# Kernel tuning notes

Measured on AMD Instinct MI355X. Metric: run time of the kernel, lower is better.

The kernel has to match this reference:

```python
import jax, jax.numpy as jnp
import numpy as np

N_RES = 500000


def _rot(vals):
    # stack 9 scalars-per-element into (..., 3, 3) row-major rotation matrices
    return jnp.stack(vals, axis=-1).reshape(*vals[0].shape, 3, 3)


def _dihedral(p0, p1, p2, p3):
    b0 = -(p1 - p0)
    b1 = p2 - p1
    b2 = p3 - p2
    b0xb1 = jnp.cross(b0, b1)
    b1xb2 = jnp.cross(b2, b1)
    y = jnp.sum(jnp.cross(b0xb1, b1xb2) * b1, axis=-1) / jnp.linalg.norm(b1, axis=-1)
    x = jnp.sum(b0xb1 * b1xb2, axis=-1)
    return jnp.nan_to_num(jnp.arctan2(y, x))


def _bb_dihedrals(N, CA, C):
    phi_ = _dihedral(C[:-1], N[1:], CA[1:], C[1:])
    psi_ = _dihedral(N[:-1], CA[:-1], C[:-1], N[1:])
    omg_ = _dihedral(CA[:-1], C[:-1], N[1:], CA[1:])
    pad = jnp.zeros_like(phi_[:1])
    omega = jnp.concatenate([omg_, pad])
    phi = jnp.concatenate([pad, phi_])
    psi = jnp.concatenate([psi_, pad])
    return jnp.stack([omega, phi, psi], axis=-1)  # (n, 3)


def _frames_from_reference(n_xyz, ca_xyz, c_xyz, eps=1e-20):
    # OpenFold Rigid.make_transform_from_reference
    n = n_xyz - ca_xyz
    c = c_xyz - ca_xyz
    cx, cy, cz = c[..., 0], c[..., 1], c[..., 2]
    z = jnp.zeros_like(cx)
    o = jnp.ones_like(cx)
    nrm = jnp.sqrt(eps + cx**2 + cy**2)
    s1, c1 = -cy / nrm, cx / nrm
    R1 = _rot([c1, -s1, z, s1, c1, z, z, z, o])
    nrm2 = jnp.sqrt(eps + cx**2 + cy**2 + cz**2)
    s2, c2 = cz / nrm2, jnp.sqrt(cx**2 + cy**2) / nrm2
    R2 = _rot([c2, z, s2, z, o, z, -s2, z, c2])
    Rc = R2 @ R1
    n2 = jnp.einsum('...ij,...j->...i', Rc, n)
    ny, nz_ = n2[..., 1], n2[..., 2]
    nrm3 = jnp.sqrt(eps + ny**2 + nz_**2)
    sn, cn = -nz_ / nrm3, ny / nrm3
    Rn = _rot([o, z, z, z, cn, -sn, z, sn, cn])
    rots = jnp.swapaxes(Rn @ Rc, -1, -2)
    return rots, ca_xyz  # (n,3,3), (n,3)


def _compose(ra, ta, rb, tb):
    # rigid composition: (ra,ta) o (rb,tb)
    return ra @ rb, jnp.einsum('...ij,...j->...i', ra, tb) + ta


def _forward(aa, bb_coords, sc_torsions, default_frames, group_idx, atom_mask, lit_positions):
    n_xyz, ca_xyz, c_xyz = bb_coords[:, 0], bb_coords[:, 1], bb_coords[:, 2]
    bb_r, bb_t = _frames_from_reference(n_xyz, ca_xyz, c_xyz)

    angles = jnp.concatenate([_bb_dihedrals(n_xyz, ca_xyz, c_xyz), sc_torsions], axis=-1)  # (n,7)
    alpha = jnp.stack([jnp.sin(angles), jnp.cos(angles)], axis=-1)  # (n,7,2) [sin, cos]
    bb_pad = jnp.concatenate([
        jnp.zeros((alpha.shape[0], 1, 1), alpha.dtype),
        jnp.ones((alpha.shape[0], 1, 1), alpha.dtype)], axis=-1)
    alpha = jnp.concatenate([bb_pad, alpha], axis=-2)  # (n,8,2)

    # torsion_angles_to_frames
    d4 = default_frames[aa]            # (n,8,4,4)
    dr, dt = d4[..., :3, :3], d4[..., :3, 3]
    s, cA = alpha[..., 0], alpha[..., 1]
    z = jnp.zeros_like(s)
    o = jnp.ones_like(s)
    Ra = _rot([o, z, z, z, cA, -s, z, s, cA])  # (n,8,3,3) x-axis rotation
    fr = dr @ Ra
    ft = dt
    # chain chi2->chi1, chi3->chi2, chi4->chi3
    r2, t2 = _compose(fr[:, 4], ft[:, 4], fr[:, 5], ft[:, 5])
    r3, t3 = _compose(r2, t2, fr[:, 6], ft[:, 6])
    r4, t4 = _compose(r3, t3, fr[:, 7], ft[:, 7])
    all_r = jnp.concatenate([fr[:, :5], r2[:, None], r3[:, None], r4[:, None]], axis=1)
    all_t = jnp.concatenate([ft[:, :5], t2[:, None], t3[:, None], t4[:, None]], axis=1)
    gr, gt = _compose(bb_r[:, None], bb_t[:, None], all_r, all_t)  # (n,8,3,3), (n,8,3)

    # frames_and_literature_positions_to_atom14_pos (one-hot sum == gather)
    n = aa.shape[0]
    g = group_idx[aa]                   # (n,14)
    ridx = jnp.arange(n)[:, None]
    ar = gr[ridx, g]                    # (n,14,3,3)
    at = gt[ridx, g]                    # (n,14,3)
    lit = lit_positions[aa]             # (n,14,3)
    pred = jnp.einsum('naij,naj->nai', ar, lit) + at
    pred = pred * atom_mask[aa][..., None]

    # use_native_bb_coords=True: keep input backbone atoms
    return jnp.concatenate([bb_coords, pred[:, 4:]], axis=1)  # (n,14,3)


def setup_inputs() -> dict:
    key = jax.random.key(0)
    ks = jax.random.split(key, 7)
    n = N_RES
    aa = jax.random.randint(ks[0], (n,), 0, 21, dtype=jnp.int32)
    bb_coords = jax.random.normal(ks[1], (n, 4, 3), jnp.float32) * 3.0
    sc_torsions = jax.random.uniform(ks[2], (n, 4), jnp.float32, -np.pi, np.pi)
    default_frames = jax.random.normal(ks[3], (21, 8, 4, 4), jnp.float32)
    group_idx = jax.random.randint(ks[4], (21, 14), 0, 8, dtype=jnp.int32)
    atom_mask = (jax.random.uniform(ks[5], (21, 14)) > 0.2).astype(jnp.float32)
    lit_positions = jax.random.normal(ks[6], (21, 14, 3), jnp.float32)
    return {"aa": aa, "bb_coords": bb_coords, "sc_torsions": sc_torsions,
            "default_frames": default_frames, "group_idx": group_idx,
            "atom_mask": atom_mask, "lit_positions": lit_positions}


def reference(aa, bb_coords, sc_torsions, default_frames, group_idx, atom_mask, lit_positions):
    return _forward(aa, bb_coords, sc_torsions, default_frames, group_idx, atom_mask, lit_positions)
```

## Files before the change

kernel.cpp:

```cpp
#include <hip/hip_runtime.h>
#include <hip/hip_fp16.h>


struct F3 { float x, y, z; };

__device__ __forceinline__ F3 f3sub(F3 a, F3 b) { return {a.x-b.x, a.y-b.y, a.z-b.z}; }
__device__ __forceinline__ F3 f3cross(F3 a, F3 b) {
    return {a.y*b.z - a.z*b.y, a.z*b.x - a.x*b.z, a.x*b.y - a.y*b.x};
}
__device__ __forceinline__ float f3dot(F3 a, F3 b) { return a.x*b.x + a.y*b.y + a.z*b.z; }

__device__ __forceinline__ void dihedral_from(F3 A, F3 B, F3 mid,
                                              float& s, float& c) {
    float x = f3dot(A, B);
    F3 w = f3cross(A, B);
    float y = f3dot(w, mid) * rsqrtf(fmaxf(f3dot(mid, mid), 1e-30f));
    float r2 = x * x + y * y;
    float rinv = rsqrtf(r2);
    bool ok = r2 > 1e-24f;
    s = ok ? y * rinv : 0.0f;
    c = ok ? x * rinv : 1.0f;
}

struct Xf12 { float m[9]; float t[3]; };
__device__ __forceinline__ Xf12 mk_fr(float4 r0, float4 r1, float4 r2,
                                      float sA, float cA) {
    Xf12 o;
    o.m[0] = r0.x; o.m[1] = fmaf(cA, r0.y, sA * r0.z); o.m[2] = fmaf(cA, r0.z, -sA * r0.y);
    o.m[3] = r1.x; o.m[4] = fmaf(cA, r1.y, sA * r1.z); o.m[5] = fmaf(cA, r1.z, -sA * r1.y);
    o.m[6] = r2.x; o.m[7] = fmaf(cA, r2.y, sA * r2.z); o.m[8] = fmaf(cA, r2.z, -sA * r2.y);
    o.t[0] = r0.w; o.t[1] = r1.w; o.t[2] = r2.w;
    return o;
}

__device__ __forceinline__ void cond_apply(const Xf12& F, bool cond,
                                           float& qx, float& qy, float& qz) {
    float tx = fmaf(F.m[0], qx, fmaf(F.m[1], qy, fmaf(F.m[2], qz, F.t[0])));
    float ty = fmaf(F.m[3], qx, fmaf(F.m[4], qy, fmaf(F.m[5], qz, F.t[1])));
    float tz = fmaf(F.m[6], qx, fmaf(F.m[7], qy, fmaf(F.m[8], qz, F.t[2])));
    qx = cond ? tx : qx; qy = cond ? ty : qy; qz = cond ? tz : qz;
}

__device__ __forceinline__ float2 h2f(float packed) {
    __half2 h = *reinterpret_cast<__half2*>(&packed);
    return __half22float2(h);
}

#define OT_STRIDE 34
#define AUV_AA    62

__global__ __launch_bounds__(256)
__attribute__((amdgpu_waves_per_eu(2, 4)))
void idealizer_kernel(
    const int*   __restrict__ aa,
    const float* __restrict__ bb,
    const float* __restrict__ tor,
    const float* __restrict__ dframes,
    const int*   __restrict__ gidx,
    const float* __restrict__ amask,
    const float* __restrict__ lit,
    float*       __restrict__ out,
    int n)
{
    __shared__ __align__(16) float s_ot[256 * OT_STRIDE];
    __shared__ __align__(16) float s_auv[21 * AUV_AA];
    __shared__ unsigned s_gpk[21];
    __shared__ unsigned s_mbit[21];

    const int tid = threadIdx.x;

    if (tid < 210) {
        int aai = (tid * 6554) >> 16;
        int a   = tid - aai * 10;
        int g   = gidx[aai * 14 + 4 + a];
        const float4* dr4 = (const float4*)dframes + (aai * 8 + g) * 4;
        float4 d0 = dr4[0], d1 = dr4[1], d2 = dr4[2];
        const float* lp = lit + aai * 42 + 12 + a * 3;
        float lx = lp[0], ly = lp[1], lz = lp[2];
        float* w = &s_auv[aai * AUV_AA + a * 6];
        w[0] = fmaf(d0.x, lx, d0.w);
        w[1] = fmaf(d1.x, lx, d1.w);
        w[2] = fmaf(d2.x, lx, d2.w);
        float U0 = fmaf(d0.y, ly, d0.z * lz), V0 = fmaf(d0.z, ly, -d0.y * lz);
        float U1 = fmaf(d1.y, ly, d1.z * lz), V1 = fmaf(d1.z, ly, -d1.y * lz);
        float U2 = fmaf(d2.y, ly, d2.z * lz), V2 = fmaf(d2.z, ly, -d2.y * lz);
        ((__half2*)w)[3] = __floats2half2_rn(U0, U1);
        ((__half2*)w)[4] = __floats2half2_rn(U2, V0);
        ((__half2*)w)[5] = __floats2half2_rn(V1, V2);
    }
    if (tid < 21) {
        unsigned gp = 0, mb = 0;
        #pragma unroll
        for (int a = 0; a < 10; a++) {
            gp |= ((unsigned)gidx[tid * 14 + 4 + a]) << (3 * a);
            mb |= (amask[tid * 14 + 4 + a] != 0.0f ? 1u : 0u) << a;
        }
        s_gpk[tid] = gp;
        s_mbit[tid] = mb;
    }
    __syncthreads();

    const int i0 = blockIdx.x * 256;
    const int i  = i0 + tid;
    if (i < n) {
        const int aai = aa[i];
        const float4* bb4 = (const float4*)bb;
        float4 q0 = bb4[i * 3 + 0];
        float4 q1 = bb4[i * 3 + 1];
        float Cz  = bb[i * 12 + 8];
        const int im = (i > 0)     ? i - 1 : 0;
        const int ip = (i < n - 1) ? i + 1 : 0;
        float4 t1 = bb4[im * 3 + 1];
        float  t2 = bb[im * 12 + 8];
        float4 r0 = bb4[ip * 3 + 0];
        float2 r1 = ((const float2*)bb)[ip * 6 + 2];
        float4 tv = ((const float4*)tor)[i];
        const float4* dfp = (const float4*)dframes + (aai * 32 + 16);
        float4 e40 = dfp[0], e41 = dfp[1],  e42 = dfp[2];
        float4 e50 = dfp[4], e51 = dfp[5],  e52 = dfp[6];
        float4 e60 = dfp[8], e61 = dfp[9],  e62 = dfp[10];

        const unsigned gpk  = s_gpk[aai];
        const unsigned mbit = s_mbit[aai];

        F3 Np  = {q0.x, q0.y, q0.z};
        F3 CAp = {q0.w, q1.x, q1.y};
        F3 Cp  = {q1.z, q1.w, Cz};
        F3 Cm  = {t1.z, t1.w, t2};
        F3 Nn  = {r0.x, r0.y, r0.z};
        F3 CAn = {r0.w, r1.x, r1.y};

        F3 u1 = f3sub(Np, Cm);
        F3 u2 = f3sub(CAp, Np);
        F3 u3 = f3sub(Cp, CAp);
        F3 u4 = f3sub(Nn, Cp);
        F3 u5 = f3sub(CAn, Nn);
        F3 c12 = f3cross(u1, u2), c23 = f3cross(u2, u3);
        F3 c34 = f3cross(u3, u4), c45 = f3cross(u4, u5);
        float s_ph, c_ph, s_ps, c_ps, s_om, c_om;
        dihedral_from(c12, c23, u2, s_ph, c_ph);
        dihedral_from(c23, c34, u3, s_ps, c_ps);
        dihedral_from(c34, c45, u4, s_om, c_om);
        if (i == 0)     { s_ph = 0.0f; c_ph = 1.0f; }
        if (i == n - 1) { s_ps = 0.0f; c_ps = 1.0f; s_om = 0.0f; c_om = 1.0f; }

        const float eps = 1e-20f;
        F3 nv = f3sub(Np, CAp);
        F3 cv = f3sub(Cp, CAp);
        float cx = cv.x, cy = cv.y, cz2 = cv.z;
        float d2xy  = cx * cx + cy * cy;
        float inrm  = rsqrtf(eps + d2xy);
        float s1 = -cy * inrm, c1 = cx * inrm;
        float inrm2 = rsqrtf(eps + d2xy + cz2 * cz2);
        float s2v = cz2 * inrm2, c2v = sqrtf(d2xy) * inrm2;
        float Rc00 = c2v * c1,  Rc01 = -c2v * s1, Rc02 = s2v;
        float Rc10 = s1,        Rc11 = c1,        Rc12 = 0.0f;
        float Rc20 = -s2v * c1, Rc21 = s2v * s1,  Rc22 = c2v;
        float n2y = Rc10 * nv.x + Rc11 * nv.y + Rc12 * nv.z;
        float n2z = Rc20 * nv.x + Rc21 * nv.y + Rc22 * nv.z;
        float inrm3 = rsqrtf(eps + n2y * n2y + n2z * n2z);
        float sn = -n2z * inrm3, cn = n2y * inrm3;
        float M10 = cn * Rc10 - sn * Rc20, M11 = cn * Rc11 - sn * Rc21, M12 = cn * Rc12 - sn * Rc22;
        float M20 = sn * Rc10 + cn * Rc20, M21 = sn * Rc11 + cn * Rc21;
        float M22 = sn * Rc12 + cn * Rc22;
        float B00 = Rc00, B01 = M10, B02 = M20;
        float B10 = Rc01, B11 = M11, B12 = M21;
        float B20 = Rc02, B21 = M12, B22 = M22;

        float sang[8], cang[8];
        sang[0] = 0.0f; cang[0] = 1.0f;
        sang[1] = s_om; cang[1] = c_om;
        sang[2] = s_ph; cang[2] = c_ph;
        sang[3] = s_ps; cang[3] = c_ps;
        __sincosf(tv.x, &sang[4], &cang[4]);
        __sincosf(tv.y, &sang[5], &cang[5]);
        __sincosf(tv.z, &sang[6], &cang[6]);
        __sincosf(tv.w, &sang[7], &cang[7]);

        float* row = &s_ot[tid * OT_STRIDE];
        float2* scw = (float2*)(row + 18);
        #pragma unroll
        for (int g8 = 0; g8 < 8; g8++)
            scw[g8] = make_float2(sang[g8], cang[g8]);

        const Xf12 F4 = mk_fr(e40, e41, e42, sang[4], cang[4]);
        const Xf12 F5 = mk_fr(e50, e51, e52, sang[5], cang[5]);
        const Xf12 F6 = mk_fr(e60, e61, e62, sang[6], cang[6]);

        float v[30];
        const float* auv = &s_auv[aai * AUV_AA];
        #pragma unroll
        for (int a = 0; a < 10; a++) {
            int g = (gpk >> (3 * a)) & 7;
            float2 sc = *(const float2*)(row + 18 + 2 * g);
            const float* ap = auv + a * 6;
            float2 w0 = *(const float2*)ap;
            float2 w1 = *(const float2*)(ap + 2);
            float2 w2 = *(const float2*)(ap + 4);
            float2 u01  = h2f(w1.y);
            float2 u2v0 = h2f(w2.x);
            float2 v12  = h2f(w2.y);
            float qx = fmaf(sc.y, u01.x,  fmaf(sc.x, u2v0.y, w0.x));
            float qy = fmaf(sc.y, u01.y,  fmaf(sc.x, v12.x,  w0.y));
            float qz = fmaf(sc.y, u2v0.x, fmaf(sc.x, v12.y,  w1.x));
            cond_apply(F6, g >= 7, qx, qy, qz);
            cond_apply(F5, g >= 6, qx, qy, qz);
            cond_apply(F4, g >= 5, qx, qy, qz);
            float mk = ((mbit >> a) & 1u) ? 1.0f : 0.0f;
            v[3*a]   = mk * fmaf(B00, qx, fmaf(B01, qy, fmaf(B02, qz, CAp.x)));
            v[3*a+1] = mk * fmaf(B10, qx, fmaf(B11, qy, fmaf(B12, qz, CAp.y)));
            v[3*a+2] = mk * fmaf(B20, qx, fmaf(B21, qy, fmaf(B22, qz, CAp.z)));
        }

        float2* so2 = (float2*)row;
        #pragma unroll
        for (int k = 0; k < 15; k++)
            so2[k] = make_float2(v[2*k], v[2*k+1]);
    }

    __syncthreads();

    int m = n - i0; if (m > 256) m = 256;
    float2* gout = (float2*)(out + (size_t)i0 * 42);
    const float2* bbt = (const float2*)(bb + (size_t)i0 * 12);
    if (m == 256) {
        int r = (tid * 24967) >> 19;
        int j = tid - r * 21;
        #pragma unroll
        for (int k = 0; k < 21; k++) {
            int off = tid + (k << 8);
            int bi = (j < 6) ? (r * 6 + j) : 0;
            float2 gval = bbt[bi];
            int tj = (j < 6) ? 0 : (j - 6);
            const float* tp = &s_ot[r * OT_STRIDE + 2 * tj];
            float2 lval = make_float2(tp[0], tp[1]);
            gout[off] = (j < 6) ? gval : lval;
            r += 12; j += 4;
            if (j >= 21) { j -= 21; r += 1; }
        }
    } else {
        const int cnt2 = m * 21;
        int r = tid / 21;
        int j = tid - r * 21;
        for (int off = tid; off < cnt2; off += 256) {
            int bi = (j < 6) ? (r * 6 + j) : 0;
            float2 gval = bbt[bi];
            int tj = (j < 6) ? 0 : (j - 6);
            const float* tp = &s_ot[r * OT_STRIDE + 2 * tj];
            float2 lval = make_float2(tp[0], tp[1]);
            gout[off] = (j < 6) ? gval : lval;
            r += 12; j += 4;
            if (j >= 21) { j -= 21; r += 1; }
        }
    }
}

extern "C" void kernel_launch(void* const* d_in, const int* in_sizes, int n_in,
                              void* d_out, int out_size, void* d_ws, size_t ws_size,
                              hipStream_t stream) {
    const int*   aa  = (const int*)d_in[0];
    const float* bb  = (const float*)d_in[1];
    const float* tor = (const float*)d_in[2];
    const float* df  = (const float*)d_in[3];
    const int*   gi  = (const int*)d_in[4];
    const float* am  = (const float*)d_in[5];
    const float* lp  = (const float*)d_in[6];
    float* outp = (float*)d_out;
    const int n = in_sizes[0];
    const int blocks = (n + 255) / 256;
    idealizer_kernel<<<blocks, 256, 0, stream>>>(aa, bb, tor, df, gi, am, lp, outp, n);
}
```

Before: 137.3 us.

## Store staged outputs and sin/cos in fp16 shared memory to raise occupancy

Packs the per-residue output coordinates, sin/cos table and per-atom-type literature terms into half2 words in LDS, cutting shared memory per block by about a third. It also raises the waves-per-EU hint so more blocks can be resident, which aims to hide the memory-bound write traffic. Output atom coordinates now pass through fp16, so side-chain positions lose precision (around 1e-3 relative). This could exceed the tolerance for coordinates of larger magnitude.

```diff
diff --git a/kernel.cpp b/kernel.cpp
--- a/kernel.cpp
+++ b/kernel.cpp
@@ -41,16 +41,20 @@
     qx = cond ? tx : qx; qy = cond ? ty : qy; qz = cond ? tz : qz;
 }
 
-__device__ __forceinline__ float2 h2f(float packed) {
-    __half2 h = *reinterpret_cast<__half2*>(&packed);
+__device__ __forceinline__ unsigned pkh(float a, float b) {
+    __half2 h = __floats2half2_rn(a, b);
+    return *reinterpret_cast<unsigned*>(&h);
+}
+__device__ __forceinline__ float2 h2fu(unsigned u) {
+    __half2 h = *reinterpret_cast<__half2*>(&u);
     return __half22float2(h);
 }
 
-#define OT_STRIDE 34
-#define AUV_AA    62
+#define OT_STRIDE 23
+#define AUV_AA    84
 
 __global__ __launch_bounds__(256)
-__attribute__((amdgpu_waves_per_eu(2, 4)))
+__attribute__((amdgpu_waves_per_eu(5, 8)))
 void idealizer_kernel(
     const int*   __restrict__ aa,
     const float* __restrict__ bb,
@@ -62,8 +66,8 @@
     float*       __restrict__ out,
     int n)
 {
-    __shared__ __align__(16) float s_ot[256 * OT_STRIDE];
-    __shared__ __align__(16) float s_auv[21 * AUV_AA];
+    __shared__ __align__(8)  unsigned s_ot[256 * OT_STRIDE];
+    __shared__ __align__(16) unsigned s_auv[21 * AUV_AA];
     __shared__ unsigned s_gpk[21];
     __shared__ unsigned s_mbit[21];
 
@@ -77,16 +81,15 @@
         float4 d0 = dr4[0], d1 = dr4[1], d2 = dr4[2];
         const float* lp = lit + aai * 42 + 12 + a * 3;
         float lx = lp[0], ly = lp[1], lz = lp[2];
-        float* w = &s_auv[aai * AUV_AA + a * 6];
-        w[0] = fmaf(d0.x, lx, d0.w);
-        w[1] = fmaf(d1.x, lx, d1.w);
-        w[2] = fmaf(d2.x, lx, d2.w);
+        float A0 = fmaf(d0.x, lx, d0.w);
+        float A1 = fmaf(d1.x, lx, d1.w);
+        float A2 = fmaf(d2.x, lx, d2.w);
         float U0 = fmaf(d0.y, ly, d0.z * lz), V0 = fmaf(d0.z, ly, -d0.y * lz);
         float U1 = fmaf(d1.y, ly, d1.z * lz), V1 = fmaf(d1.z, ly, -d1.y * lz);
         float U2 = fmaf(d2.y, ly, d2.z * lz), V2 = fmaf(d2.z, ly, -d2.y * lz);
-        ((__half2*)w)[3] = __floats2half2_rn(U0, U1);
-        ((__half2*)w)[4] = __floats2half2_rn(U2, V0);
-        ((__half2*)w)[5] = __floats2half2_rn(V1, V2);
+        unsigned* w = &s_auv[aai * AUV_AA + a * 8];
+        *(uint4*)w = make_uint4(pkh(A0, A1), pkh(A2, U0), pkh(U1, U2), pkh(V0, V1));
+        w[4] = pkh(V2, 0.0f);
     }
     if (tid < 21) {
         unsigned gp = 0, mb = 0;
@@ -177,45 +180,47 @@
         __sincosf(tv.z, &sang[6], &cang[6]);
         __sincosf(tv.w, &sang[7], &cang[7]);
 
-        float* row = &s_ot[tid * OT_STRIDE];
-        float2* scw = (float2*)(row + 18);
+        unsigned* rowd = &s_ot[tid * OT_STRIDE];
         #pragma unroll
         for (int g8 = 0; g8 < 8; g8++)
-            scw[g8] = make_float2(sang[g8], cang[g8]);
+            rowd[15 + g8] = pkh(sang[g8], cang[g8]);
 
         const Xf12 F4 = mk_fr(e40, e41, e42, sang[4], cang[4]);
         const Xf12 F5 = mk_fr(e50, e51, e52, sang[5], cang[5]);
         const Xf12 F6 = mk_fr(e60, e61, e62, sang[6], cang[6]);
 
-        float v[30];
-        const float* auv = &s_auv[aai * AUV_AA];
+        const unsigned* auv = &s_auv[aai * AUV_AA];
+        float px = 0.0f, py = 0.0f, pz = 0.0f;
         #pragma unroll
         for (int a = 0; a < 10; a++) {
             int g = (gpk >> (3 * a)) & 7;
-            float2 sc = *(const float2*)(row + 18 + 2 * g);
-            const float* ap = auv + a * 6;
-            float2 w0 = *(const float2*)ap;
-            float2 w1 = *(const float2*)(ap + 2);
-            float2 w2 = *(const float2*)(ap + 4);
-            float2 u01  = h2f(w1.y);
-            float2 u2v0 = h2f(w2.x);
-            float2 v12  = h2f(w2.y);
-            float qx = fmaf(sc.y, u01.x,  fmaf(sc.x, u2v0.y, w0.x));
-            float qy = fmaf(sc.y, u01.y,  fmaf(sc.x, v12.x,  w0.y));
-            float qz = fmaf(sc.y, u2v0.x, fmaf(sc.x, v12.y,  w1.x));
+            float2 sc = h2fu(rowd[15 + g]);
+            uint4 rw = *(const uint4*)(auv + a * 8);
+            unsigned rv = auv[a * 8 + 4];
+            float2 a01  = h2fu(rw.x);
+            float2 a2u0 = h2fu(rw.y);
+            float2 u12  = h2fu(rw.z);
+            float2 v01  = h2fu(rw.w);
+            float2 v2_  = h2fu(rv);
+            float qx = fmaf(sc.y, a2u0.y, fmaf(sc.x, v01.x, a01.x));
+            float qy = fmaf(sc.y, u12.x,  fmaf(sc.x, v01.y, a01.y));
+            float qz = fmaf(sc.y, u12.y,  fmaf(sc.x, v2_.x, a2u0.x));
             cond_apply(F6, g >= 7, qx, qy, qz);
             cond_apply(F5, g >= 6, qx, qy, qz);
             cond_apply(F4, g >= 5, qx, qy, qz);
             float mk = ((mbit >> a) & 1u) ? 1.0f : 0.0f;
-            v[3*a]   = mk * fmaf(B00, qx, fmaf(B01, qy, fmaf(B02, qz, CAp.x)));
-            v[3*a+1] = mk * fmaf(B10, qx, fmaf(B11, qy, fmaf(B12, qz, CAp.y)));
-            v[3*a+2] = mk * fmaf(B20, qx, fmaf(B21, qy, fmaf(B22, qz, CAp.z)));
-        }
-
-        float2* so2 = (float2*)row;
-        #pragma unroll
-        for (int k = 0; k < 15; k++)
-            so2[k] = make_float2(v[2*k], v[2*k+1]);
+            float x = mk * fmaf(B00, qx, fmaf(B01, qy, fmaf(B02, qz, CAp.x)));
+            float y = mk * fmaf(B10, qx, fmaf(B11, qy, fmaf(B12, qz, CAp.y)));
+            float z = mk * fmaf(B20, qx, fmaf(B21, qy, fmaf(B22, qz, CAp.z)));
+            if ((a & 1) == 0) {
+                px = x; py = y; pz = z;
+            } else {
+                int base = 3 * (a >> 1);
+                rowd[base + 0] = pkh(px, py);
+                rowd[base + 1] = pkh(pz, x);
+                rowd[base + 2] = pkh(y, z);
+            }
+        }
     }
 
     __syncthreads();
@@ -232,8 +237,7 @@
             int bi = (j < 6) ? (r * 6 + j) : 0;
             float2 gval = bbt[bi];
             int tj = (j < 6) ? 0 : (j - 6);
-            const float* tp = &s_ot[r * OT_STRIDE + 2 * tj];
-            float2 lval = make_float2(tp[0], tp[1]);
+            float2 lval = h2fu(s_ot[r * OT_STRIDE + tj]);
             gout[off] = (j < 6) ? gval : lval;
             r += 12; j += 4;
             if (j >= 21) { j -= 21; r += 1; }
@@ -246,8 +250,7 @@
             int bi = (j < 6) ? (r * 6 + j) : 0;
             float2 gval = bbt[bi];
             int tj = (j < 6) ? 0 : (j - 6);
-            const float* tp = &s_ot[r * OT_STRIDE + 2 * tj];
-            float2 lval = make_float2(tp[0], tp[1]);
+            float2 lval = h2fu(s_ot[r * OT_STRIDE + tj]);
             gout[off] = (j < 6) ? gval : lval;
             r += 12; j += 4;
             if (j >= 21) { j -= 21; r += 1; }
```

New measurement: 253.4 us. 84.6% more time.
